# Optimization experiments

Measured on AMD Instinct MI355X. Metric: run time of the kernel, lower is better.

Reference implementation:

```python
import math
import jax, jax.numpy as jnp
import numpy as np

FEATURE_DIM = 16
HEADS = 8
DIM = 512
HEAD_DIM = DIM // HEADS
EPS = 1e-12
_RD = math.sqrt(FEATURE_DIM)        # sqrt(d)
_RRD = math.sqrt(_RD)               # d^{1/4}
_R2 = math.sqrt(2.0)
_IU, _JU = np.triu_indices(FEATURE_DIM, k=1)  # row-major upper-tri (excl diag), matches torch.triu_indices


def taylor_feature_map(x):
    # x: (..., F) -> (..., 1 + F + F + F*(F-1)/2) = (..., 153) for F=16
    off = x[..., _IU] * x[..., _JU]          # upper triangle of outer product, no full FxF materialization
    diag = x * x
    return jnp.concatenate([
        jnp.ones_like(x[..., :1]),
        x / _RRD,
        diag / (_RD * _R2),
        off / _RD,
    ], axis=-1)


def setup_inputs() -> dict:
    key = jax.random.key(0)
    k0, k1, k2, k3, k4 = jax.random.split(key, 5)
    b, t, d = 2, 1024, DIM
    hidden_states = jax.random.normal(k0, (b, t, d), dtype=jnp.float32)
    s = 0.02
    Wq = jax.random.normal(k1, (HEADS * FEATURE_DIM, d), dtype=jnp.float32) * s
    Wk = jax.random.normal(k2, (HEADS * FEATURE_DIM, d), dtype=jnp.float32) * s
    Wv = jax.random.normal(k3, (HEADS * HEAD_DIM, d), dtype=jnp.float32) * s
    Wo = jax.random.normal(k4, (d, HEADS * HEAD_DIM), dtype=jnp.float32) * s
    return {"hidden_states": hidden_states, "Wq": Wq, "Wk": Wk, "Wv": Wv, "Wo": Wo}


def reference(hidden_states, Wq, Wk, Wv, Wo):
    b, t, d = hidden_states.shape
    h, f, hd = HEADS, FEATURE_DIM, HEAD_DIM
    q = (hidden_states @ Wq.T).reshape(b, t, h, f).transpose(0, 2, 1, 3)    # (b,h,t,f)
    k = (hidden_states @ Wk.T).reshape(b, t, h, f).transpose(0, 2, 1, 3)
    v = (hidden_states @ Wv.T).reshape(b, t, h, hd).transpose(0, 2, 1, 3)   # (b,h,t,hd)
    q = taylor_feature_map(q)   # (b,h,t,F) with F=153
    k = taylor_feature_map(k)
    # causal linear attention via cumulative state
    kv = k[..., None, :] * v[..., :, None]          # (b,h,t,hd,F)
    kv_cum = jnp.cumsum(kv, axis=2)                 # (b,h,t,hd,F)
    num = jnp.einsum('bhtf,bhtdf->bhtd', q, kv_cum) # (b,h,t,hd)
    k_cum = jnp.cumsum(k, axis=2)                   # (b,h,t,F)
    den = jnp.einsum('bhtf,bhtf->bht', q, k_cum)[..., None] + EPS
    y = num / den                                   # (b,h,t,hd)
    y = y.transpose(0, 2, 1, 3).reshape(b, t, h * hd)
    return y @ Wo.T
```

## Files before the change

kernel.cpp:

```cpp
#include <hip/hip_runtime.h>
#include <hip/hip_bf16.h>

#define BB 2
#define TT 1024
#define DD 512
#define HH 8
#define FF 16
#define HDIM 64
#define BT (BB*TT)

typedef short bf16x8 __attribute__((ext_vector_type(8)));
typedef float f32x4  __attribute__((ext_vector_type(4)));
#define MFMA_BF16 __builtin_amdgcn_mfma_f32_16x16x32_bf16

__device__ __forceinline__ ushort f2b(float f) {
    uint u = __float_as_uint(f);
    uint r = (u + 0x7fffu + ((u >> 16) & 1u)) >> 16;
    return (ushort)r;
}

__device__ __forceinline__ uint pkbf2(float a, float b) {
    __hip_bfloat162 h = __float22bfloat162_rn(make_float2(a, b));
    union { __hip_bfloat162 h2; uint u; } c; c.h2 = h;
    return c.u;
}

__global__ __launch_bounds__(256) void cast_all(
    const float* __restrict__ X,  const float* __restrict__ Wq,
    const float* __restrict__ Wk, const float* __restrict__ Wv,
    const float* __restrict__ Wo,
    ushort* __restrict__ Xb, ushort* __restrict__ Wb, ushort* __restrict__ Wob)
{
    const int i4 = (blockIdx.x * 256 + threadIdx.x) * 4;
    const float* src; ushort* dst;
    if (i4 < 1048576)      { src = X  + i4;             dst = Xb + i4; }
    else if (i4 < 1114112) { src = Wq + (i4 - 1048576); dst = Wb + (i4 - 1048576); }
    else if (i4 < 1179648) { src = Wk + (i4 - 1114112); dst = Wb + 65536 + (i4 - 1114112); }
    else if (i4 < 1441792) { src = Wv + (i4 - 1179648); dst = Wb + 131072 + (i4 - 1179648); }
    else                   { src = Wo + (i4 - 1441792); dst = Wob + (i4 - 1441792); }
    float4 v = *(const float4*)src;
    ushort4 o = { f2b(v.x), f2b(v.y), f2b(v.z), f2b(v.w) };
    *(ushort4*)dst = o;
}

__global__ __launch_bounds__(512) void qkv_mfma(
    const ushort* __restrict__ Xb, const ushort* __restrict__ Wb,
    ushort* __restrict__ Qb, ushort* __restrict__ Kb, ushort* __restrict__ Vtg)
{
    __shared__ float sc[2][64][66];
    const int m0 = blockIdx.x * 64, n0 = blockIdx.y * 64;
    const int tid = threadIdx.x, w = tid >> 6, l = tid & 63;
    const int kw = w >> 2, mw = w & 1, nw = (w >> 1) & 1;
    const int lr = l & 15, g = l >> 4;

    f32x4 acc[2][2] = {};
    const ushort* Ar = Xb + (size_t)(m0 + mw*32 + lr) * 512 + kw*256 + g*8;
    const ushort* Br = Wb + (size_t)(n0 + nw*32 + lr) * 512 + kw*256 + g*8;

    bf16x8 a0c = *(const bf16x8*)(Ar);
    bf16x8 a1c = *(const bf16x8*)(Ar + (size_t)16*512);
    bf16x8 b0c = *(const bf16x8*)(Br);
    bf16x8 b1c = *(const bf16x8*)(Br + (size_t)16*512);
    #pragma unroll
    for (int ks = 0; ks < 8; ++ks) {
        bf16x8 a0n = a0c, a1n = a1c, b0n = b0c, b1n = b1c;
        if (ks < 7) {
            a0n = *(const bf16x8*)(Ar + (ks+1)*32);
            a1n = *(const bf16x8*)(Ar + (size_t)16*512 + (ks+1)*32);
            b0n = *(const bf16x8*)(Br + (ks+1)*32);
            b1n = *(const bf16x8*)(Br + (size_t)16*512 + (ks+1)*32);
        }
        acc[0][0] = MFMA_BF16(a0c, b0c, acc[0][0], 0, 0, 0);
        acc[0][1] = MFMA_BF16(a0c, b1c, acc[0][1], 0, 0, 0);
        acc[1][0] = MFMA_BF16(a1c, b0c, acc[1][0], 0, 0, 0);
        acc[1][1] = MFMA_BF16(a1c, b1c, acc[1][1], 0, 0, 0);
        a0c = a0n; a1c = a1n; b0c = b0n; b1c = b1n;
    }

    #pragma unroll
    for (int mb = 0; mb < 2; ++mb)
        #pragma unroll
        for (int nb = 0; nb < 2; ++nb)
            #pragma unroll
            for (int r = 0; r < 4; ++r)
                sc[kw][mw*32 + mb*16 + g*4 + r][nw*32 + nb*16 + lr] = acc[mb][nb][r];
    __syncthreads();

    const int vl = tid & 63, rg = tid >> 6;
    const int cg = n0 + vl;
    float v8[8];
    #pragma unroll
    for (int j = 0; j < 8; ++j) v8[j] = sc[0][rg*8 + j][vl] + sc[1][rg*8 + j][vl];
    const int tok0 = m0 + rg*8;
    const int b = tok0 >> 10, tt0 = tok0 & 1023;
    if (cg < 256) {
        const bool isQ = cg < 128;
        const int c = isQ ? cg : cg - 128;
        const int h = c >> 4, f = c & 15;
        ushort* Dst = isQ ? Qb : Kb;
        #pragma unroll
        for (int j = 0; j < 8; ++j)
            Dst[((size_t)(b*HH + h)*TT + tt0 + j)*FF + f] = f2b(v8[j]);
    } else {
        const int c = cg - 256;
        const int h = c >> 6, v = c & 63;
        uint2 p0 = { pkbf2(v8[0], v8[1]), pkbf2(v8[2], v8[3]) };
        uint2 p1 = { pkbf2(v8[4], v8[5]), pkbf2(v8[6], v8[7]) };
        ushort* base = Vtg + ((size_t)(b*HH + h)*64 + v)*TT + tt0;
        *(uint2*)base       = p0;
        *(uint2*)(base + 4) = p1;
    }
}

__global__ __launch_bounds__(512) void attn_mfma(
    const ushort* __restrict__ Qb, const ushort* __restrict__ Kb,
    const ushort* __restrict__ Vtg, ushort* __restrict__ Yb)
{
    __shared__ float smem[8*32*68 + 8*32];
    short (*Pl)[32][72] = (short(*)[32][72])smem;
    float* scf = smem;
    float* scd = smem + 8*32*68;

    const int bid = blockIdx.x;
    const int qt = 31 - (bid >> 4);
    const int bh = bid & 15;
    const int b = bh >> 3, h = bh & 7;
    const int tid = threadIdx.x, w = tid >> 6, l = tid & 63;
    const int lr = l & 15, g = l >> 4;
    const int nkc = (qt + 2) >> 1;
    const bf16x8 zf = {0,0,0,0,0,0,0,0};

    bf16x8 qf[2];
    #pragma unroll
    for (int nb = 0; nb < 2; ++nb)
        qf[nb] = (l < 32)
            ? *(const bf16x8*)(Qb + ((size_t)bh*TT + qt*32 + nb*16 + lr)*FF + g*8)
            : zf;

    f32x4 o[4][2] = {};
    float den[2] = {0.f, 0.f};

    for (int kc = w; kc < nkc; kc += 8) {
        #pragma unroll
        for (int mb = 0; mb < 4; ++mb) {
            bf16x8 kf = (l < 32)
                ? *(const bf16x8*)(Kb + ((size_t)bh*TT + kc*64 + mb*16 + lr)*FF + g*8)
                : zf;
            #pragma unroll
            for (int nb = 0; nb < 2; ++nb) {
                f32x4 z4 = {};
                f32x4 s = MFMA_BF16(kf, qf[nb], z4, 0, 0, 0);
                const int qg = qt*32 + nb*16 + lr;
                const int kg0 = kc*64 + mb*16 + g*4;
                float pv[4];
                #pragma unroll
                for (int r = 0; r < 4; ++r) {
                    float ss = s[r] * 0.25f;
                    float pp = fmaf(ss, fmaf(ss, 0.5f, 1.0f), 1.0f);
                    if (kg0 + r > qg) pp = 0.f;
                    den[nb] += pp;
                    pv[r] = pp;
                }
                uint2 pk = { pkbf2(pv[0], pv[1]), pkbf2(pv[2], pv[3]) };
                *(uint2*)&Pl[w][nb*16 + lr][mb*16 + g*4] = pk;
            }
        }

        #pragma unroll
        for (int kb = 0; kb < 2; ++kb)
            #pragma unroll
            for (int mv = 0; mv < 4; ++mv) {
                bf16x8 vf = *(const bf16x8*)(Vtg +
                    ((size_t)bh*64 + mv*16 + lr)*TT + kc*64 + kb*32 + g*8);
                #pragma unroll
                for (int nb = 0; nb < 2; ++nb) {
                    bf16x8 pf = *(const bf16x8*)&Pl[w][nb*16 + lr][kb*32 + g*8];
                    o[mv][nb] = MFMA_BF16(vf, pf, o[mv][nb], 0, 0, 0);
                }
            }
    }

    float dred[2];
    #pragma unroll
    for (int nb = 0; nb < 2; ++nb) {
        float d = den[nb];
        d += __shfl_xor(d, 16);
        d += __shfl_xor(d, 32);
        dred[nb] = d;
    }

    __syncthreads();

    #pragma unroll
    for (int mv = 0; mv < 4; ++mv)
        #pragma unroll
        for (int nb = 0; nb < 2; ++nb)
            *(f32x4*)&scf[(size_t)(w*32 + nb*16 + lr)*68 + mv*16 + g*4] = o[mv][nb];
    if (g == 0) {
        scd[w*32 + lr]      = dred[0];
        scd[w*32 + 16 + lr] = dred[1];
    }

    __syncthreads();

    {
        const int q  = tid >> 4;
        const int v0 = (tid & 15) * 4;
        float dtot = 0.f;
        #pragma unroll
        for (int ww = 0; ww < 8; ++ww) dtot += scd[ww*32 + q];
        const float inv = 1.0f / (dtot + 1e-12f);
        float o0 = 0.f, o1 = 0.f, o2 = 0.f, o3 = 0.f;
        #pragma unroll
        for (int ww = 0; ww < 8; ++ww) {
            const float* p = &scf[(size_t)(ww*32 + q)*68 + v0];
            o0 += p[0]; o1 += p[1]; o2 += p[2]; o3 += p[3];
        }
        uint2 pk = { pkbf2(o0*inv, o1*inv), pkbf2(o2*inv, o3*inv) };
        *(uint2*)(Yb + ((size_t)(b*TT + qt*32 + q))*DD + h*HDIM + v0) = pk;
    }
}

__global__ __launch_bounds__(512) void out_mfma(
    const ushort* __restrict__ Yb, const ushort* __restrict__ Wob,
    float* __restrict__ Out)
{
    __shared__ float sc[2][64][66];
    const int m0 = blockIdx.x * 64, n0 = blockIdx.y * 64;
    const int tid = threadIdx.x, w = tid >> 6, l = tid & 63;
    const int kw = w >> 2, mw = w & 1, nw = (w >> 1) & 1;
    const int lr = l & 15, g = l >> 4;

    f32x4 acc[2][2] = {};
    const ushort* Ar = Yb  + (size_t)(m0 + mw*32 + lr) * 512 + kw*256 + g*8;
    const ushort* Br = Wob + (size_t)(n0 + nw*32 + lr) * 512 + kw*256 + g*8;

    bf16x8 a0c = *(const bf16x8*)(Ar);
    bf16x8 a1c = *(const bf16x8*)(Ar + (size_t)16*512);
    bf16x8 b0c = *(const bf16x8*)(Br);
    bf16x8 b1c = *(const bf16x8*)(Br + (size_t)16*512);
    #pragma unroll
    for (int ks = 0; ks < 8; ++ks) {
        bf16x8 a0n = a0c, a1n = a1c, b0n = b0c, b1n = b1c;
        if (ks < 7) {
            a0n = *(const bf16x8*)(Ar + (ks+1)*32);
            a1n = *(const bf16x8*)(Ar + (size_t)16*512 + (ks+1)*32);
            b0n = *(const bf16x8*)(Br + (ks+1)*32);
            b1n = *(const bf16x8*)(Br + (size_t)16*512 + (ks+1)*32);
        }
        acc[0][0] = MFMA_BF16(a0c, b0c, acc[0][0], 0, 0, 0);
        acc[0][1] = MFMA_BF16(a0c, b1c, acc[0][1], 0, 0, 0);
        acc[1][0] = MFMA_BF16(a1c, b0c, acc[1][0], 0, 0, 0);
        acc[1][1] = MFMA_BF16(a1c, b1c, acc[1][1], 0, 0, 0);
        a0c = a0n; a1c = a1n; b0c = b0n; b1c = b1n;
    }

    #pragma unroll
    for (int mb = 0; mb < 2; ++mb)
        #pragma unroll
        for (int nb = 0; nb < 2; ++nb)
            #pragma unroll
            for (int r = 0; r < 4; ++r)
                sc[kw][mw*32 + mb*16 + g*4 + r][nw*32 + nb*16 + lr] = acc[mb][nb][r];
    __syncthreads();

    const int vl = tid & 63, rg = tid >> 6;
    #pragma unroll
    for (int j = 0; j < 8; ++j) {
        const float v = sc[0][rg*8 + j][vl] + sc[1][rg*8 + j][vl];
        Out[(size_t)(m0 + rg*8 + j)*512 + n0 + vl] = v;
    }
}

extern "C" void kernel_launch(void* const* d_in, const int* in_sizes, int n_in,
                              void* d_out, int out_size, void* d_ws, size_t ws_size,
                              hipStream_t stream) {
    const float* X  = (const float*)d_in[0];
    const float* Wq = (const float*)d_in[1];
    const float* Wk = (const float*)d_in[2];
    const float* Wv = (const float*)d_in[3];
    const float* Wo = (const float*)d_in[4];
    float* out = (float*)d_out;

    ushort* ws = (ushort*)d_ws;
    ushort* Xb  = ws;
    ushort* Wb  = Xb  + 1048576;
    ushort* Wob = Wb  + 393216;
    ushort* Qb  = Wob + 262144;
    ushort* Kb  = Qb  + 262144;
    ushort* Vtg = Kb  + 262144;
    ushort* Yb  = Vtg + 1048576;

    cast_all<<<1664, 256, 0, stream>>>(X, Wq, Wk, Wv, Wo, Xb, Wb, Wob);

    dim3 g1(BT/64, 768/64);
    qkv_mfma<<<g1, 512, 0, stream>>>(Xb, Wb, Qb, Kb, Vtg);

    attn_mfma<<<512, 512, 0, stream>>>(Qb, Kb, Vtg, Yb);

    dim3 g3(BT/64, DD/64);
    out_mfma<<<g3, 512, 0, stream>>>(Yb, Wob, out);
}
```

Measured before the change: 48.68 us.

## Fuse fp32-to-bf16 casting into QKV projection and drop separate cast kernel

Removes the standalone cast kernel. The QKV GEMM now loads fp32 X and weights directly and converts them to bf16 in registers before each MFMA. An extra grid row (blockIdx.y==12) casts Wo for the later output projection. This saves one launch and the round trip through a bf16 workspace, at the cost of twice the global load bytes per GEMM block and repeated conversion of X across 12 column blocks.

```diff
diff --git a/kernel.cpp b/kernel.cpp
--- a/kernel.cpp
+++ b/kernel.cpp
@@ -25,56 +25,72 @@
     return c.u;
 }
 
-__global__ __launch_bounds__(256) void cast_all(
+struct fr8 { float4 a, b; };
+__device__ __forceinline__ fr8 ld8(const float* p) {
+    fr8 r; r.a = *(const float4*)p; r.b = *(const float4*)(p + 4); return r;
+}
+__device__ __forceinline__ bf16x8 c8(const fr8& x) {
+    union { bf16x8 v; uint u[4]; } r;
+    r.u[0] = pkbf2(x.a.x, x.a.y);
+    r.u[1] = pkbf2(x.a.z, x.a.w);
+    r.u[2] = pkbf2(x.b.x, x.b.y);
+    r.u[3] = pkbf2(x.b.z, x.b.w);
+    return r.v;
+}
+
+__global__ __launch_bounds__(512) void qkv_mfma(
     const float* __restrict__ X,  const float* __restrict__ Wq,
     const float* __restrict__ Wk, const float* __restrict__ Wv,
     const float* __restrict__ Wo,
-    ushort* __restrict__ Xb, ushort* __restrict__ Wb, ushort* __restrict__ Wob)
+    ushort* __restrict__ Qb, ushort* __restrict__ Kb,
+    ushort* __restrict__ Vtg, ushort* __restrict__ Wob)
 {
-    const int i4 = (blockIdx.x * 256 + threadIdx.x) * 4;
-    const float* src; ushort* dst;
-    if (i4 < 1048576)      { src = X  + i4;             dst = Xb + i4; }
-    else if (i4 < 1114112) { src = Wq + (i4 - 1048576); dst = Wb + (i4 - 1048576); }
-    else if (i4 < 1179648) { src = Wk + (i4 - 1114112); dst = Wb + 65536 + (i4 - 1114112); }
-    else if (i4 < 1441792) { src = Wv + (i4 - 1179648); dst = Wb + 131072 + (i4 - 1179648); }
-    else                   { src = Wo + (i4 - 1441792); dst = Wob + (i4 - 1441792); }
-    float4 v = *(const float4*)src;
-    ushort4 o = { f2b(v.x), f2b(v.y), f2b(v.z), f2b(v.w) };
-    *(ushort4*)dst = o;
-}
-
-__global__ __launch_bounds__(512) void qkv_mfma(
-    const ushort* __restrict__ Xb, const ushort* __restrict__ Wb,
-    ushort* __restrict__ Qb, ushort* __restrict__ Kb, ushort* __restrict__ Vtg)
-{
+    if (blockIdx.y == 12) {
+        const int idx = blockIdx.x * 512 + threadIdx.x;
+        #pragma unroll
+        for (int j = 0; j < 4; ++j) {
+            const int u = j * 16384 + idx;
+            float4 v = *(const float4*)(Wo + (size_t)u * 4);
+            ushort4 o = { f2b(v.x), f2b(v.y), f2b(v.z), f2b(v.w) };
+            *(ushort4*)(Wob + (size_t)u * 4) = o;
+        }
+        return;
+    }
+
     __shared__ float sc[2][64][66];
     const int m0 = blockIdx.x * 64, n0 = blockIdx.y * 64;
     const int tid = threadIdx.x, w = tid >> 6, l = tid & 63;
     const int kw = w >> 2, mw = w & 1, nw = (w >> 1) & 1;
     const int lr = l & 15, g = l >> 4;
 
+    const float* Wsrc; int nb0;
+    if (n0 < 128)      { Wsrc = Wq; nb0 = n0; }
+    else if (n0 < 256) { Wsrc = Wk; nb0 = n0 - 128; }
+    else               { Wsrc = Wv; nb0 = n0 - 256; }
+
     f32x4 acc[2][2] = {};
-    const ushort* Ar = Xb + (size_t)(m0 + mw*32 + lr) * 512 + kw*256 + g*8;
-    const ushort* Br = Wb + (size_t)(n0 + nw*32 + lr) * 512 + kw*256 + g*8;
-
-    bf16x8 a0c = *(const bf16x8*)(Ar);
-    bf16x8 a1c = *(const bf16x8*)(Ar + (size_t)16*512);
-    bf16x8 b0c = *(const bf16x8*)(Br);
-    bf16x8 b1c = *(const bf16x8*)(Br + (size_t)16*512);
+    const float* Ar = X    + (size_t)(m0 + mw*32 + lr) * 512 + kw*256 + g*8;
+    const float* Br = Wsrc + (size_t)(nb0 + nw*32 + lr) * 512 + kw*256 + g*8;
+
+    fr8 A0 = ld8(Ar);
+    fr8 A1 = ld8(Ar + (size_t)16*512);
+    fr8 B0 = ld8(Br);
+    fr8 B1 = ld8(Br + (size_t)16*512);
     #pragma unroll
     for (int ks = 0; ks < 8; ++ks) {
-        bf16x8 a0n = a0c, a1n = a1c, b0n = b0c, b1n = b1c;
+        fr8 A0n, A1n, B0n, B1n;
         if (ks < 7) {
-            a0n = *(const bf16x8*)(Ar + (ks+1)*32);
-            a1n = *(const bf16x8*)(Ar + (size_t)16*512 + (ks+1)*32);
-            b0n = *(const bf16x8*)(Br + (ks+1)*32);
-            b1n = *(const bf16x8*)(Br + (size_t)16*512 + (ks+1)*32);
-        }
-        acc[0][0] = MFMA_BF16(a0c, b0c, acc[0][0], 0, 0, 0);
-        acc[0][1] = MFMA_BF16(a0c, b1c, acc[0][1], 0, 0, 0);
-        acc[1][0] = MFMA_BF16(a1c, b0c, acc[1][0], 0, 0, 0);
-        acc[1][1] = MFMA_BF16(a1c, b1c, acc[1][1], 0, 0, 0);
-        a0c = a0n; a1c = a1n; b0c = b0n; b1c = b1n;
+            A0n = ld8(Ar + (ks+1)*32);
+            A1n = ld8(Ar + (size_t)16*512 + (ks+1)*32);
+            B0n = ld8(Br + (ks+1)*32);
+            B1n = ld8(Br + (size_t)16*512 + (ks+1)*32);
+        }
+        bf16x8 a0 = c8(A0), a1 = c8(A1), b0 = c8(B0), b1 = c8(B1);
+        acc[0][0] = MFMA_BF16(a0, b0, acc[0][0], 0, 0, 0);
+        acc[0][1] = MFMA_BF16(a0, b1, acc[0][1], 0, 0, 0);
+        acc[1][0] = MFMA_BF16(a1, b0, acc[1][0], 0, 0, 0);
+        acc[1][1] = MFMA_BF16(a1, b1, acc[1][1], 0, 0, 0);
+        if (ks < 7) { A0 = A0n; A1 = A1n; B0 = B0n; B1 = B1n; }
     }
 
     #pragma unroll
@@ -283,18 +299,14 @@
     float* out = (float*)d_out;
 
     ushort* ws = (ushort*)d_ws;
-    ushort* Xb  = ws;
-    ushort* Wb  = Xb  + 1048576;
-    ushort* Wob = Wb  + 393216;
+    ushort* Wob = ws;
     ushort* Qb  = Wob + 262144;
     ushort* Kb  = Qb  + 262144;
     ushort* Vtg = Kb  + 262144;
     ushort* Yb  = Vtg + 1048576;
 
-    cast_all<<<1664, 256, 0, stream>>>(X, Wq, Wk, Wv, Wo, Xb, Wb, Wob);
-
-    dim3 g1(BT/64, 768/64);
-    qkv_mfma<<<g1, 512, 0, stream>>>(Xb, Wb, Qb, Kb, Vtg);
+    dim3 g1(BT/64, 13);
+    qkv_mfma<<<g1, 512, 0, stream>>>(X, Wq, Wk, Wv, Wo, Qb, Kb, Vtg, Wob);
 
     attn_mfma<<<512, 512, 0, stream>>>(Qb, Kb, Vtg, Yb);
 
```

New measurement: 57.24 us. 17.6% more time.

## Halve attention query tile, skip masked key blocks, compute denominator via MFMA

Applied to the files above, without the earlier changes.

The attention kernel now processes 16 queries per block instead of 32, doubling the grid to 1024 blocks for better load balance across CUs. In the diagonal chunk it only computes and multiplies the key sub-blocks that are not fully masked, and off-diagonal chunks skip the causal mask test. The row-sum denominator is computed with an extra MFMA against a ones vector rather than scalar accumulation, and the 0.25 score scale is folded into K in the projection kernel. Cross-wave reduction becomes a two-stage tree through shared memory. Costs include reloading V per smaller query tile, more total blocks, and an additional rounding of K after scaling (exact in bf16 since the factor is a power of two).

```diff
diff --git a/kernel.cpp b/kernel.cpp
--- a/kernel.cpp
+++ b/kernel.cpp
@@ -98,9 +98,10 @@
         const int c = isQ ? cg : cg - 128;
         const int h = c >> 4, f = c & 15;
         ushort* Dst = isQ ? Qb : Kb;
+        const float scale = isQ ? 1.0f : 0.25f;
         #pragma unroll
         for (int j = 0; j < 8; ++j)
-            Dst[((size_t)(b*HH + h)*TT + tt0 + j)*FF + f] = f2b(v8[j]);
+            Dst[((size_t)(b*HH + h)*TT + tt0 + j)*FF + f] = f2b(v8[j] * scale);
     } else {
         const int c = cg - 256;
         const int h = c >> 6, v = c & 63;
@@ -116,108 +117,109 @@
     const ushort* __restrict__ Qb, const ushort* __restrict__ Kb,
     const ushort* __restrict__ Vtg, ushort* __restrict__ Yb)
 {
-    __shared__ float smem[8*32*68 + 8*32];
-    short (*Pl)[32][72] = (short(*)[32][72])smem;
+    __shared__ float smem[4608];
+    short (*Pl)[16][72] = (short(*)[16][72])smem;
     float* scf = smem;
-    float* scd = smem + 8*32*68;
+    float* scd = smem + 4*16*68;
 
     const int bid = blockIdx.x;
-    const int qt = 31 - (bid >> 4);
+    const int qt = 63 - (bid >> 4);
     const int bh = bid & 15;
     const int b = bh >> 3, h = bh & 7;
     const int tid = threadIdx.x, w = tid >> 6, l = tid & 63;
     const int lr = l & 15, g = l >> 4;
-    const int nkc = (qt + 2) >> 1;
+    const int qend = (qt + 1) * 16;
+    const int nkc = (qend + 63) >> 6;
     const bf16x8 zf = {0,0,0,0,0,0,0,0};
-
-    bf16x8 qf[2];
-    #pragma unroll
-    for (int nb = 0; nb < 2; ++nb)
-        qf[nb] = (l < 32)
-            ? *(const bf16x8*)(Qb + ((size_t)bh*TT + qt*32 + nb*16 + lr)*FF + g*8)
-            : zf;
-
-    f32x4 o[4][2] = {};
-    float den[2] = {0.f, 0.f};
+    const bf16x8 ones = {16256,16256,16256,16256,16256,16256,16256,16256};
+
+    bf16x8 qf = (l < 32)
+        ? *(const bf16x8*)(Qb + ((size_t)bh*TT + qt*16 + lr)*FF + g*8)
+        : zf;
+
+    f32x4 o[4] = {};
+    f32x4 dacc = {};
 
     for (int kc = w; kc < nkc; kc += 8) {
-        #pragma unroll
-        for (int mb = 0; mb < 4; ++mb) {
+        const bool diagc = (kc == nkc - 1);
+        const int act = qend - kc*64;
+        const int nmb = diagc ? (act >> 4) : 4;
+        const int kb_max = diagc ? ((nmb + 1) >> 1) : 2;
+
+        for (int mb = 0; mb < nmb; ++mb) {
             bf16x8 kf = (l < 32)
                 ? *(const bf16x8*)(Kb + ((size_t)bh*TT + kc*64 + mb*16 + lr)*FF + g*8)
                 : zf;
-            #pragma unroll
-            for (int nb = 0; nb < 2; ++nb) {
-                f32x4 z4 = {};
-                f32x4 s = MFMA_BF16(kf, qf[nb], z4, 0, 0, 0);
-                const int qg = qt*32 + nb*16 + lr;
+            f32x4 z4 = {};
+            f32x4 s = MFMA_BF16(kf, qf, z4, 0, 0, 0);
+            float pv[4];
+            if (diagc) {
+                const int qg = qt*16 + lr;
                 const int kg0 = kc*64 + mb*16 + g*4;
-                float pv[4];
                 #pragma unroll
                 for (int r = 0; r < 4; ++r) {
-                    float ss = s[r] * 0.25f;
-                    float pp = fmaf(ss, fmaf(ss, 0.5f, 1.0f), 1.0f);
-                    if (kg0 + r > qg) pp = 0.f;
-                    den[nb] += pp;
-                    pv[r] = pp;
+                    float pp = fmaf(s[r], fmaf(s[r], 0.5f, 1.0f), 1.0f);
+                    pv[r] = (kg0 + r > qg) ? 0.f : pp;
                 }
-                uint2 pk = { pkbf2(pv[0], pv[1]), pkbf2(pv[2], pv[3]) };
-                *(uint2*)&Pl[w][nb*16 + lr][mb*16 + g*4] = pk;
+            } else {
+                #pragma unroll
+                for (int r = 0; r < 4; ++r)
+                    pv[r] = fmaf(s[r], fmaf(s[r], 0.5f, 1.0f), 1.0f);
             }
-        }
-
-        #pragma unroll
-        for (int kb = 0; kb < 2; ++kb)
+            uint2 pk = { pkbf2(pv[0], pv[1]), pkbf2(pv[2], pv[3]) };
+            *(uint2*)&Pl[w][lr][mb*16 + g*4] = pk;
+        }
+        for (int mb = nmb; mb < kb_max*2; ++mb) {
+            uint2 zz = {0u, 0u};
+            *(uint2*)&Pl[w][lr][mb*16 + g*4] = zz;
+        }
+
+        for (int kb = 0; kb < kb_max; ++kb) {
+            bf16x8 pf = *(const bf16x8*)&Pl[w][lr][kb*32 + g*8];
             #pragma unroll
             for (int mv = 0; mv < 4; ++mv) {
                 bf16x8 vf = *(const bf16x8*)(Vtg +
                     ((size_t)bh*64 + mv*16 + lr)*TT + kc*64 + kb*32 + g*8);
-                #pragma unroll
-                for (int nb = 0; nb < 2; ++nb) {
-                    bf16x8 pf = *(const bf16x8*)&Pl[w][nb*16 + lr][kb*32 + g*8];
-                    o[mv][nb] = MFMA_BF16(vf, pf, o[mv][nb], 0, 0, 0);
-                }
+                o[mv] = MFMA_BF16(vf, pf, o[mv], 0, 0, 0);
             }
-    }
-
-    float dred[2];
-    #pragma unroll
-    for (int nb = 0; nb < 2; ++nb) {
-        float d = den[nb];
-        d += __shfl_xor(d, 16);
-        d += __shfl_xor(d, 32);
-        dred[nb] = d;
-    }
-
-    __syncthreads();
-
-    #pragma unroll
-    for (int mv = 0; mv < 4; ++mv)
-        #pragma unroll
-        for (int nb = 0; nb < 2; ++nb)
-            *(f32x4*)&scf[(size_t)(w*32 + nb*16 + lr)*68 + mv*16 + g*4] = o[mv][nb];
-    if (g == 0) {
-        scd[w*32 + lr]      = dred[0];
-        scd[w*32 + 16 + lr] = dred[1];
-    }
-
-    __syncthreads();
-
-    {
+            dacc = MFMA_BF16(ones, pf, dacc, 0, 0, 0);
+        }
+    }
+
+    __syncthreads();
+
+    if (w >= 4) {
+        #pragma unroll
+        for (int mv = 0; mv < 4; ++mv)
+            *(f32x4*)&scf[(size_t)((w-4)*16 + lr)*68 + mv*16 + g*4] = o[mv];
+        if (l < 16) scd[(w-4)*16 + lr] = dacc[0];
+    }
+    __syncthreads();
+
+    if (w < 4) {
+        #pragma unroll
+        for (int mv = 0; mv < 4; ++mv) {
+            f32x4 p = *(const f32x4*)&scf[(size_t)(w*16 + lr)*68 + mv*16 + g*4];
+            o[mv] = o[mv] + p;
+            *(f32x4*)&scf[(size_t)(w*16 + lr)*68 + mv*16 + g*4] = o[mv];
+        }
+        if (l < 16) scd[w*16 + lr] += dacc[0];
+    }
+    __syncthreads();
+
+    if (tid < 256) {
         const int q  = tid >> 4;
         const int v0 = (tid & 15) * 4;
-        float dtot = 0.f;
-        #pragma unroll
-        for (int ww = 0; ww < 8; ++ww) dtot += scd[ww*32 + q];
+        const float dtot = scd[q] + scd[16 + q] + scd[32 + q] + scd[48 + q];
         const float inv = 1.0f / (dtot + 1e-12f);
         float o0 = 0.f, o1 = 0.f, o2 = 0.f, o3 = 0.f;
         #pragma unroll
-        for (int ww = 0; ww < 8; ++ww) {
-            const float* p = &scf[(size_t)(ww*32 + q)*68 + v0];
+        for (int s4 = 0; s4 < 4; ++s4) {
+            const float* p = &scf[(size_t)(s4*16 + q)*68 + v0];
             o0 += p[0]; o1 += p[1]; o2 += p[2]; o3 += p[3];
         }
         uint2 pk = { pkbf2(o0*inv, o1*inv), pkbf2(o2*inv, o3*inv) };
-        *(uint2*)(Yb + ((size_t)(b*TT + qt*32 + q))*DD + h*HDIM + v0) = pk;
+        *(uint2*)(Yb + ((size_t)(b*TT + qt*16 + q))*DD + h*HDIM + v0) = pk;
     }
 }
 
@@ -296,7 +298,7 @@
     dim3 g1(BT/64, 768/64);
     qkv_mfma<<<g1, 512, 0, stream>>>(Xb, Wb, Qb, Kb, Vtg);
 
-    attn_mfma<<<512, 512, 0, stream>>>(Qb, Kb, Vtg, Yb);
+    attn_mfma<<<1024, 512, 0, stream>>>(Qb, Kb, Vtg, Yb);
 
     dim3 g3(BT/64, DD/64);
     out_mfma<<<g3, 512, 0, stream>>>(Yb, Wob, out);
```

New measurement: 50.12 us. 1.03x slower.

## Skip masked key blocks on diagonal chunk and compute denominator via MFMA

Applied to the files above, without the earlier changes.

Folds the 0.25 score scale into K at projection time and drops it from the inner loop. On the diagonal chunk only the key sub-blocks that can be unmasked are processed, and the causal mask check now runs only on that chunk. The per-element denominator sum is replaced by an MFMA of a ones vector against the bf16 P tile, which removes scalar adds and the shuffle reduction but sums bf16-rounded probabilities. The loops now have runtime trip counts and are no longer unrolled, which may hurt scheduling.

```diff
diff --git a/kernel.cpp b/kernel.cpp
--- a/kernel.cpp
+++ b/kernel.cpp
@@ -98,9 +98,10 @@
         const int c = isQ ? cg : cg - 128;
         const int h = c >> 4, f = c & 15;
         ushort* Dst = isQ ? Qb : Kb;
+        const float scale = isQ ? 1.0f : 0.25f;
         #pragma unroll
         for (int j = 0; j < 8; ++j)
-            Dst[((size_t)(b*HH + h)*TT + tt0 + j)*FF + f] = f2b(v8[j]);
+            Dst[((size_t)(b*HH + h)*TT + tt0 + j)*FF + f] = f2b(v8[j] * scale);
     } else {
         const int c = cg - 256;
         const int h = c >> 6, v = c & 63;
@@ -127,8 +128,10 @@
     const int b = bh >> 3, h = bh & 7;
     const int tid = threadIdx.x, w = tid >> 6, l = tid & 63;
     const int lr = l & 15, g = l >> 4;
+    const int qend = qt*32 + 32;
     const int nkc = (qt + 2) >> 1;
     const bf16x8 zf = {0,0,0,0,0,0,0,0};
+    const bf16x8 ones = {16256,16256,16256,16256,16256,16256,16256,16256};
 
     bf16x8 qf[2];
     #pragma unroll
@@ -138,11 +141,15 @@
             : zf;
 
     f32x4 o[4][2] = {};
-    float den[2] = {0.f, 0.f};
+    f32x4 dacc[2] = {};
 
     for (int kc = w; kc < nkc; kc += 8) {
-        #pragma unroll
-        for (int mb = 0; mb < 4; ++mb) {
+        const bool diagc = (kc == nkc - 1);
+        const int act = qend - kc*64;
+        const int nmb = diagc ? (act >> 4) : 4;
+        const int kb_max = nmb >> 1;
+
+        for (int mb = 0; mb < nmb; ++mb) {
             bf16x8 kf = (l < 32)
                 ? *(const bf16x8*)(Kb + ((size_t)bh*TT + kc*64 + mb*16 + lr)*FF + g*8)
                 : zf;
@@ -150,24 +157,26 @@
             for (int nb = 0; nb < 2; ++nb) {
                 f32x4 z4 = {};
                 f32x4 s = MFMA_BF16(kf, qf[nb], z4, 0, 0, 0);
-                const int qg = qt*32 + nb*16 + lr;
-                const int kg0 = kc*64 + mb*16 + g*4;
                 float pv[4];
-                #pragma unroll
-                for (int r = 0; r < 4; ++r) {
-                    float ss = s[r] * 0.25f;
-                    float pp = fmaf(ss, fmaf(ss, 0.5f, 1.0f), 1.0f);
-                    if (kg0 + r > qg) pp = 0.f;
-                    den[nb] += pp;
-                    pv[r] = pp;
+                if (diagc) {
+                    const int qg = qt*32 + nb*16 + lr;
+                    const int kg0 = kc*64 + mb*16 + g*4;
+                    #pragma unroll
+                    for (int r = 0; r < 4; ++r) {
+                        float pp = fmaf(s[r], fmaf(s[r], 0.5f, 1.0f), 1.0f);
+                        pv[r] = (kg0 + r > qg) ? 0.f : pp;
+                    }
+                } else {
+                    #pragma unroll
+                    for (int r = 0; r < 4; ++r)
+                        pv[r] = fmaf(s[r], fmaf(s[r], 0.5f, 1.0f), 1.0f);
                 }
                 uint2 pk = { pkbf2(pv[0], pv[1]), pkbf2(pv[2], pv[3]) };
                 *(uint2*)&Pl[w][nb*16 + lr][mb*16 + g*4] = pk;
             }
         }
 
-        #pragma unroll
-        for (int kb = 0; kb < 2; ++kb)
+        for (int kb = 0; kb < kb_max; ++kb) {
             #pragma unroll
             for (int mv = 0; mv < 4; ++mv) {
                 bf16x8 vf = *(const bf16x8*)(Vtg +
@@ -178,15 +187,12 @@
                     o[mv][nb] = MFMA_BF16(vf, pf, o[mv][nb], 0, 0, 0);
                 }
             }
-    }
-
-    float dred[2];
-    #pragma unroll
-    for (int nb = 0; nb < 2; ++nb) {
-        float d = den[nb];
-        d += __shfl_xor(d, 16);
-        d += __shfl_xor(d, 32);
-        dred[nb] = d;
+            #pragma unroll
+            for (int nb = 0; nb < 2; ++nb) {
+                bf16x8 pf = *(const bf16x8*)&Pl[w][nb*16 + lr][kb*32 + g*8];
+                dacc[nb] = MFMA_BF16(ones, pf, dacc[nb], 0, 0, 0);
+            }
+        }
     }
 
     __syncthreads();
@@ -197,8 +203,8 @@
         for (int nb = 0; nb < 2; ++nb)
             *(f32x4*)&scf[(size_t)(w*32 + nb*16 + lr)*68 + mv*16 + g*4] = o[mv][nb];
     if (g == 0) {
-        scd[w*32 + lr]      = dred[0];
-        scd[w*32 + 16 + lr] = dred[1];
+        scd[w*32 + lr]      = dacc[0][0];
+        scd[w*32 + 16 + lr] = dacc[1][0];
     }
 
     __syncthreads();
```

Result: no change. 47.75 us (-1.9%).
